# Kernel tuning notes

Measured on AMD Instinct MI355X. Metric: run time of the kernel, lower is better.

Reference implementation:

```python
import jax, jax.numpy as jnp
import numpy as np

N, LN, S, T = 50000, 64, 8, 4
E = 800000
MU = 0.9


def setup_inputs() -> dict:
    key = jax.random.key(0)
    ks = jax.random.split(key, 10)
    X_Node = jax.random.randint(ks[0], (E,), 0, N, dtype=jnp.int64) if jax.config.jax_enable_x64 else jax.random.randint(ks[0], (E,), 0, N).astype(jnp.int32)
    X_Neis = jax.random.randint(ks[1], (E,), 0, N).astype(X_Node.dtype)
    dg_list = jax.random.randint(ks[2], (E,), 1, 64).astype(jnp.float32)
    sc = 0.05
    W_emb = jax.random.normal(ks[3], (N, LN), jnp.float32) * sc
    Wxi = jax.random.normal(ks[4], (2 * LN, S * S), jnp.float32) * sc
    bxi = jnp.zeros((S * S,), jnp.float32)
    Wrou = jax.random.normal(ks[5], (LN, S), jnp.float32) * sc
    brou = jnp.zeros((S,), jnp.float32)
    Wout = jax.random.normal(ks[6], (LN + S, 3), jnp.float32) * sc
    bout = jnp.zeros((3,), jnp.float32)
    return {"X_Node": X_Node, "X_Neis": X_Neis, "dg_list": dg_list,
            "W_emb": W_emb, "Wxi": Wxi, "bxi": bxi,
            "Wrou": Wrou, "brou": brou, "Wout": Wout, "bout": bout}


def reference(X_Node, X_Neis, dg_list, W_emb, Wxi, bxi, Wrou, brou, Wout, bout):
    # Edge-wise feature gather: X = [emb[src] || emb[dst]]  -> [E, 2*LN]
    node_e = W_emb[X_Node]
    neis_e = W_emb[X_Neis]
    X = jnp.concatenate([node_e, neis_e], axis=1)
    # Hw precompute (loop-invariant): A [E,S,S], b [E,S]
    A = jnp.tanh(X @ Wxi + bxi).reshape(-1, S, S) * (MU / S) / dg_list[:, None, None]
    b = jnp.tanh(node_e @ Wrou + brou)

    states = jnp.zeros((N, S), dtype=W_emb.dtype)

    def step(states, _):
        H = states[X_Node]                      # gather [E, S]
        H = jnp.einsum('eij,ej->ei', A, H) + b  # per-edge small matvec
        # AggrSum's one-hot [V,E] matmul == scatter-add by X_Node
        new_states = jax.ops.segment_sum(H, X_Node, num_segments=N)
        return new_states, None

    states, _ = jax.lax.scan(step, states, None, length=T)
    logits = jnp.concatenate([W_emb, states], axis=1) @ Wout + bout
    return jax.nn.softmax(logits, axis=1)
```

## Files before the change

### kernel.cpp

```cpp
#include <hip/hip_runtime.h>
#include <hip/hip_fp16.h>
#include <math.h>

#define N_NODES 50000
#define LNDIM   64
#define E_EDGES 800000
#define MU_OVER_S 0.1125f
#define HPAD 16
#define NRANGE 8
#define RANGE_SZ ((N_NODES + NRANGE - 1) / NRANGE)
#define MAXDEG 48
#define PRE_TPB 128
#define PRE_TILES ((N_NODES + PRE_TPB - 1) / PRE_TPB)
#define LDS_STRIDE 129

__device__ __forceinline__ unsigned short f2bf(float f) {
    unsigned int u = __float_as_uint(f);
    u = (u + 0x7FFFu + ((u >> 16) & 1u)) >> 16;
    return (unsigned short)u;
}
__device__ __forceinline__ float bf2f(unsigned short b) {
    return __uint_as_float((unsigned)b << 16);
}
__device__ __forceinline__ float h2f(unsigned short h) {
    __half_raw hr; hr.x = h;
    return __half2float(__half(hr));
}
__device__ __forceinline__ float poly_tanh(float x) {
    float x2 = x * x;
    float a  = fmaf(x2, 0.13333333333f, -0.33333333333f);
    return fmaf(x * x2, a, x);
}

__global__ __launch_bounds__(256) void zero_kernel(int4* __restrict__ p, int n4)
{
    int i = blockIdx.x * 256 + threadIdx.x;
    if (i < n4) p[i] = make_int4(0, 0, 0, 0);
}

__global__ __launch_bounds__(PRE_TPB, 4) void precompute_kernel(
    const float* __restrict__ W_emb, const float* __restrict__ Wxi,
    const float* __restrict__ bxi,   const float* __restrict__ Wrou,
    const float* __restrict__ brou,
    unsigned short* __restrict__ T1, unsigned short* __restrict__ U,
    float* __restrict__ Bv)
{
    __shared__ float ldsT[32 * LDS_STRIDE];
    int pass = blockIdx.x / PRE_TILES;
    int tile = blockIdx.x % PRE_TILES;
    int tid  = threadIdx.x;
    int base = tile * PRE_TPB;
    int v    = base + tid;

    if (pass == 4) {
        float acc[8];
        #pragma unroll
        for (int j = 0; j < 8; ++j) acc[j] = brou[j];
        for (int kc = 0; kc < 2; ++kc) {
            __syncthreads();
            #pragma unroll
            for (int c = 0; c < 8; ++c) {
                int idx  = c * PRE_TPB + tid;
                int node = idx >> 3, part = idx & 7;
                int nn   = min(base + node, N_NODES - 1);
                float4 q = *(const float4*)(W_emb + (size_t)nn * 64 + kc * 32 + part * 4);
                ldsT[(part*4+0)*LDS_STRIDE + node] = q.x;
                ldsT[(part*4+1)*LDS_STRIDE + node] = q.y;
                ldsT[(part*4+2)*LDS_STRIDE + node] = q.z;
                ldsT[(part*4+3)*LDS_STRIDE + node] = q.w;
            }
            __syncthreads();
            for (int kk = 0; kk < 32; ++kk) {
                float ek = ldsT[kk * LDS_STRIDE + tid];
                const float* wr = Wrou + (kc*32 + kk) * 8;
                #pragma unroll
                for (int j = 0; j < 8; ++j) acc[j] = fmaf(ek, wr[j], acc[j]);
            }
        }
        if (v < N_NODES) {
            float4* dst = (float4*)(Bv + (size_t)v * 8);
            dst[0] = make_float4(tanhf(acc[0]), tanhf(acc[1]), tanhf(acc[2]), tanhf(acc[3]));
            dst[1] = make_float4(tanhf(acc[4]), tanhf(acc[5]), tanhf(acc[6]), tanhf(acc[7]));
        }
        return;
    }

    int is_u  = pass >> 1;
    int jbase = (pass & 1) * 32;
    const float* W = Wxi + (is_u ? 64 * 64 : 0) + jbase;
    float acc[32];
    if (is_u) {
        #pragma unroll
        for (int j = 0; j < 32; ++j) acc[j] = 0.f;
    } else {
        #pragma unroll
        for (int j = 0; j < 32; ++j) acc[j] = bxi[jbase + j];
    }
    for (int kc = 0; kc < 2; ++kc) {
        __syncthreads();
        #pragma unroll
        for (int c = 0; c < 8; ++c) {
            int idx  = c * PRE_TPB + tid;
            int node = idx >> 3, part = idx & 7;
            int nn   = min(base + node, N_NODES - 1);
            float4 q = *(const float4*)(W_emb + (size_t)nn * 64 + kc * 32 + part * 4);
            ldsT[(part*4+0)*LDS_STRIDE + node] = q.x;
            ldsT[(part*4+1)*LDS_STRIDE + node] = q.y;
            ldsT[(part*4+2)*LDS_STRIDE + node] = q.z;
            ldsT[(part*4+3)*LDS_STRIDE + node] = q.w;
        }
        __syncthreads();
        for (int kk = 0; kk < 32; ++kk) {
            float ek = ldsT[kk * LDS_STRIDE + tid];
            const float* wr = W + (kc*32 + kk) * 64;
            #pragma unroll
            for (int j = 0; j < 32; ++j) acc[j] = fmaf(ek, wr[j], acc[j]);
        }
    }
    if (v >= N_NODES) return;
    unsigned short* outp = is_u ? U : T1;
    uint4* dst = (uint4*)(outp + (size_t)v * 64 + jbase);
    #pragma unroll
    for (int t = 0; t < 4; ++t) {
        uint4 q;
        q.x = (unsigned)f2bf(acc[8*t+0]) | ((unsigned)f2bf(acc[8*t+1]) << 16);
        q.y = (unsigned)f2bf(acc[8*t+2]) | ((unsigned)f2bf(acc[8*t+3]) << 16);
        q.z = (unsigned)f2bf(acc[8*t+4]) | ((unsigned)f2bf(acc[8*t+5]) << 16);
        q.w = (unsigned)f2bf(acc[8*t+6]) | ((unsigned)f2bf(acc[8*t+7]) << 16);
        dst[t] = q;
    }
}

__global__ __launch_bounds__(256) void scatter_kernel(
    const int* __restrict__ X_Node, const int* __restrict__ X_Neis,
    const float* __restrict__ dg_list, int* __restrict__ cnt_arr,
    unsigned* __restrict__ pk_s)
{
    int r = blockIdx.x & (NRANGE - 1);
    int e = (blockIdx.x >> 3) * 256 + threadIdx.x;
    if (e >= E_EDGES) return;
    int node = X_Node[e];
    if (node < r * RANGE_SZ || node >= (r + 1) * RANGE_SZ) return;
    unsigned nei = (unsigned)X_Neis[e];
    float    sc  = MU_OVER_S / dg_list[e];
    __half_raw hr = __half_raw(__float2half(sc));
    unsigned hb  = (unsigned)hr.x;
    int pos = atomicAdd(&cnt_arr[(size_t)node * HPAD], 1);
    if (pos < MAXDEG) pk_s[(size_t)node * MAXDEG + pos] = nei | (hb << 16);
}

__global__ __launch_bounds__(256, 4) void main_kernel(
    const float* __restrict__ W_emb, const float* __restrict__ Wout,
    const float* __restrict__ bout,
    const unsigned short* __restrict__ T1, const unsigned short* __restrict__ U,
    const float* __restrict__ Bv, const int* __restrict__ cnt_arr,
    const unsigned* __restrict__ pk_s, float* __restrict__ out)
{
    int lane = threadIdx.x & 63;
    int wid  = threadIdx.x >> 6;
    int v    = blockIdx.x * 4 + wid;
    if (v >= N_NODES) return;

    int cntv = min(cnt_arr[(size_t)v * HPAD], MAXDEG);
    unsigned pk = (lane < MAXDEG) ? pk_s[(size_t)v * MAXDEG + lane] : 0u;
    float t = bf2f(T1[(size_t)v * 64 + lane]);

    float m0 = 0.f, m1 = 0.f, m2 = 0.f, m3 = 0.f;
    int cnt4 = (cntv + 3) & ~3;

    if (cnt4 > 0) {
        unsigned cq0 = (unsigned)__builtin_amdgcn_readlane((int)pk, 0);
        unsigned cq1 = (unsigned)__builtin_amdgcn_readlane((int)pk, 1);
        unsigned cq2 = (unsigned)__builtin_amdgcn_readlane((int)pk, 2);
        unsigned cq3 = (unsigned)__builtin_amdgcn_readlane((int)pk, 3);
        float cu0 = bf2f(U[(size_t)(cq0 & 0xFFFFu) * 64 + lane]);
        float cu1 = bf2f(U[(size_t)(cq1 & 0xFFFFu) * 64 + lane]);
        float cu2 = bf2f(U[(size_t)(cq2 & 0xFFFFu) * 64 + lane]);
        float cu3 = bf2f(U[(size_t)(cq3 & 0xFFFFu) * 64 + lane]);

        for (int k = 0; k < cnt4; k += 4) {
            int kn = (k + 4 < cnt4) ? k + 4 : 0;
            unsigned nq0 = (unsigned)__builtin_amdgcn_readlane((int)pk, kn + 0);
            unsigned nq1 = (unsigned)__builtin_amdgcn_readlane((int)pk, kn + 1);
            unsigned nq2 = (unsigned)__builtin_amdgcn_readlane((int)pk, kn + 2);
            unsigned nq3 = (unsigned)__builtin_amdgcn_readlane((int)pk, kn + 3);
            float nu0 = bf2f(U[(size_t)(nq0 & 0xFFFFu) * 64 + lane]);
            float nu1 = bf2f(U[(size_t)(nq1 & 0xFFFFu) * 64 + lane]);
            float nu2 = bf2f(U[(size_t)(nq2 & 0xFFFFu) * 64 + lane]);
            float nu3 = bf2f(U[(size_t)(nq3 & 0xFFFFu) * 64 + lane]);

            float g0 = poly_tanh(t + cu0) * h2f((unsigned short)(cq0 >> 16));
            float g1 = poly_tanh(t + cu1) * h2f((unsigned short)(cq1 >> 16));
            float g2 = poly_tanh(t + cu2) * h2f((unsigned short)(cq2 >> 16));
            float g3 = poly_tanh(t + cu3) * h2f((unsigned short)(cq3 >> 16));
            m0 += (k + 0 < cntv) ? g0 : 0.f;
            m1 += (k + 1 < cntv) ? g1 : 0.f;
            m2 += (k + 2 < cntv) ? g2 : 0.f;
            m3 += (k + 3 < cntv) ? g3 : 0.f;

            cq0 = nq0; cq1 = nq1; cq2 = nq2; cq3 = nq3;
            cu0 = nu0; cu1 = nu1; cu2 = nu2; cu3 = nu3;
        }
    }
    float macc = (m0 + m1) + (m2 + m3);

    int   j   = lane & 7;
    int   i   = lane >> 3;
    float cnt = (float)cntv;
    float cj  = cnt * Bv[v * 8 + j];
    float ci  = __shfl(cj, i);
    float sj  = cj;

    #pragma unroll
    for (int step = 0; step < 3; ++step) {
        float p = macc * sj;
        p += __shfl_xor(p, 1);
        p += __shfl_xor(p, 2);
        p += __shfl_xor(p, 4);
        float snew = p + ci;
        sj = __shfl(snew, j * 8);
    }

    float emb = W_emb[(size_t)v * 64 + lane];
    float p0 = emb * Wout[lane * 3 + 0];
    float p1 = emb * Wout[lane * 3 + 1];
    float p2 = emb * Wout[lane * 3 + 2];
    if (lane < 8) {
        p0 = fmaf(sj, Wout[(64 + lane) * 3 + 0], p0);
        p1 = fmaf(sj, Wout[(64 + lane) * 3 + 1], p1);
        p2 = fmaf(sj, Wout[(64 + lane) * 3 + 2], p2);
    }
    #pragma unroll
    for (int m = 1; m < 64; m <<= 1) {
        p0 += __shfl_xor(p0, m);
        p1 += __shfl_xor(p1, m);
        p2 += __shfl_xor(p2, m);
    }
    float L0 = p0 + bout[0], L1 = p1 + bout[1], L2 = p2 + bout[2];
    float mx = fmaxf(L0, fmaxf(L1, L2));
    float e0 = expf(L0 - mx), e1 = expf(L1 - mx), e2 = expf(L2 - mx);
    float inv = 1.f / (e0 + e1 + e2);
    float rr = (lane == 0) ? e0 : (lane == 1 ? e1 : e2);
    if (lane < 3) out[v * 3 + lane] = rr * inv;
}

extern "C" void kernel_launch(void* const* d_in, const int* in_sizes, int n_in,
                              void* d_out, int out_size, void* d_ws, size_t ws_size,
                              hipStream_t stream)
{
    const int*   X_Node = (const int*)  d_in[0];
    const int*   X_Neis = (const int*)  d_in[1];
    const float* dg     = (const float*)d_in[2];
    const float* W_emb  = (const float*)d_in[3];
    const float* Wxi    = (const float*)d_in[4];
    const float* bxi    = (const float*)d_in[5];
    const float* Wrou   = (const float*)d_in[6];
    const float* brou   = (const float*)d_in[7];
    const float* Wout   = (const float*)d_in[8];
    const float* bout   = (const float*)d_in[9];
    float*       out    = (float*)d_out;

    char*  ws  = (char*)d_ws;
    size_t off = 0;
    auto alloc = [&](size_t bytes) -> void* {
        void* p = ws + off;
        off += (bytes + 255) & ~(size_t)255;
        return p;
    };
    unsigned short* T1      = (unsigned short*)alloc((size_t)N_NODES * 64 * 2);
    unsigned short* U       = (unsigned short*)alloc((size_t)N_NODES * 64 * 2);
    float*          Bv      = (float*)alloc((size_t)N_NODES * 8 * 4);
    int*            cnt_arr = (int*)  alloc((size_t)N_NODES * HPAD * 4);
    unsigned*       pk_s    = (unsigned*)alloc(((size_t)N_NODES * MAXDEG + 64) * 4);

    const int NBE = (E_EDGES + 255) / 256;
    const int NZ4 = N_NODES * HPAD / 4;

    zero_kernel<<<(NZ4 + 255) / 256, 256, 0, stream>>>((int4*)cnt_arr, NZ4);
    precompute_kernel<<<PRE_TILES * 5, PRE_TPB, 0, stream>>>(
        W_emb, Wxi, bxi, Wrou, brou, T1, U, Bv);
    scatter_kernel<<<NBE * NRANGE, 256, 0, stream>>>(
        X_Node, X_Neis, dg, cnt_arr, pk_s);
    main_kernel<<<(N_NODES + 3) / 4, 256, 0, stream>>>(
        W_emb, Wout, bout, T1, U, Bv, cnt_arr, pk_s, out);
}
```

Baseline: 110.5 us.

## Two-pass bucketed edge scatter and 16-wide batched neighbor gathers

The edge scatter used to re-read every edge in 8 node-range passes. It now runs one bucketing pass that writes (node, payload) pairs into 8 per-range buckets using block-local LDS counts and one global atomic per bucket. A second pass does the per-node atomic placement from those buckets, which aims to cut redundant edge reads and improve atomic locality. The main kernel's gather loop now issues 16 U loads before any compute, separated by a sched_barrier, to raise memory-level parallelism at the cost of more registers. Bucket overflow past BCAP drops edges silently, and the readlane reads past cntv depend on the padded pk_s tail.

```diff
diff --git a/kernel.cpp b/kernel.cpp
--- a/kernel.cpp
+++ b/kernel.cpp
@@ -10,6 +10,7 @@
 #define NRANGE 8
 #define RANGE_SZ ((N_NODES + NRANGE - 1) / NRANGE)
 #define MAXDEG 48
+#define BCAP 110000
 #define PRE_TPB 128
 #define PRE_TILES ((N_NODES + PRE_TPB - 1) / PRE_TPB)
 #define LDS_STRIDE 129
@@ -131,22 +132,42 @@
     }
 }
 
-__global__ __launch_bounds__(256) void scatter_kernel(
+__global__ __launch_bounds__(256) void bucket_kernel(
     const int* __restrict__ X_Node, const int* __restrict__ X_Neis,
-    const float* __restrict__ dg_list, int* __restrict__ cnt_arr,
-    unsigned* __restrict__ pk_s)
-{
-    int r = blockIdx.x & (NRANGE - 1);
-    int e = (blockIdx.x >> 3) * 256 + threadIdx.x;
-    if (e >= E_EDGES) return;
+    const float* __restrict__ dg_list, int* __restrict__ bkt_cursor,
+    uint2* __restrict__ pairs)
+{
+    __shared__ int cnt[NRANGE];
+    __shared__ int basep[NRANGE];
+    int tid = threadIdx.x;
+    int e   = blockIdx.x * 256 + tid;
+    if (tid < NRANGE) cnt[tid] = 0;
+    __syncthreads();
+
     int node = X_Node[e];
-    if (node < r * RANGE_SZ || node >= (r + 1) * RANGE_SZ) return;
     unsigned nei = (unsigned)X_Neis[e];
     float    sc  = MU_OVER_S / dg_list[e];
     __half_raw hr = __half_raw(__float2half(sc));
-    unsigned hb  = (unsigned)hr.x;
-    int pos = atomicAdd(&cnt_arr[(size_t)node * HPAD], 1);
-    if (pos < MAXDEG) pk_s[(size_t)node * MAXDEG + pos] = nei | (hb << 16);
+    unsigned py  = nei | ((unsigned)hr.x << 16);
+    int r    = node / RANGE_SZ;
+    int rank = atomicAdd(&cnt[r], 1);
+    __syncthreads();
+    if (tid < NRANGE) basep[tid] = atomicAdd(&bkt_cursor[tid * HPAD], cnt[tid]);
+    __syncthreads();
+    int pos = basep[r] + rank;
+    if (pos < BCAP) pairs[(size_t)r * BCAP + pos] = make_uint2((unsigned)node, py);
+}
+
+__global__ __launch_bounds__(256) void scatter2_kernel(
+    const uint2* __restrict__ pairs, const int* __restrict__ bkt_cursor,
+    int* __restrict__ cnt_arr, unsigned* __restrict__ pk_s)
+{
+    int r = blockIdx.x & (NRANGE - 1);
+    int i = (blockIdx.x >> 3) * 256 + threadIdx.x;
+    if (i >= bkt_cursor[r * HPAD]) return;
+    uint2 p = pairs[(size_t)r * BCAP + i];
+    int pos = atomicAdd(&cnt_arr[(size_t)p.x * HPAD], 1);
+    if (pos < MAXDEG) pk_s[(size_t)p.x * MAXDEG + pos] = p.y;
 }
 
 __global__ __launch_bounds__(256, 4) void main_kernel(
@@ -166,40 +187,24 @@
     float t = bf2f(T1[(size_t)v * 64 + lane]);
 
     float m0 = 0.f, m1 = 0.f, m2 = 0.f, m3 = 0.f;
-    int cnt4 = (cntv + 3) & ~3;
-
-    if (cnt4 > 0) {
-        unsigned cq0 = (unsigned)__builtin_amdgcn_readlane((int)pk, 0);
-        unsigned cq1 = (unsigned)__builtin_amdgcn_readlane((int)pk, 1);
-        unsigned cq2 = (unsigned)__builtin_amdgcn_readlane((int)pk, 2);
-        unsigned cq3 = (unsigned)__builtin_amdgcn_readlane((int)pk, 3);
-        float cu0 = bf2f(U[(size_t)(cq0 & 0xFFFFu) * 64 + lane]);
-        float cu1 = bf2f(U[(size_t)(cq1 & 0xFFFFu) * 64 + lane]);
-        float cu2 = bf2f(U[(size_t)(cq2 & 0xFFFFu) * 64 + lane]);
-        float cu3 = bf2f(U[(size_t)(cq3 & 0xFFFFu) * 64 + lane]);
-
-        for (int k = 0; k < cnt4; k += 4) {
-            int kn = (k + 4 < cnt4) ? k + 4 : 0;
-            unsigned nq0 = (unsigned)__builtin_amdgcn_readlane((int)pk, kn + 0);
-            unsigned nq1 = (unsigned)__builtin_amdgcn_readlane((int)pk, kn + 1);
-            unsigned nq2 = (unsigned)__builtin_amdgcn_readlane((int)pk, kn + 2);
-            unsigned nq3 = (unsigned)__builtin_amdgcn_readlane((int)pk, kn + 3);
-            float nu0 = bf2f(U[(size_t)(nq0 & 0xFFFFu) * 64 + lane]);
-            float nu1 = bf2f(U[(size_t)(nq1 & 0xFFFFu) * 64 + lane]);
-            float nu2 = bf2f(U[(size_t)(nq2 & 0xFFFFu) * 64 + lane]);
-            float nu3 = bf2f(U[(size_t)(nq3 & 0xFFFFu) * 64 + lane]);
-
-            float g0 = poly_tanh(t + cu0) * h2f((unsigned short)(cq0 >> 16));
-            float g1 = poly_tanh(t + cu1) * h2f((unsigned short)(cq1 >> 16));
-            float g2 = poly_tanh(t + cu2) * h2f((unsigned short)(cq2 >> 16));
-            float g3 = poly_tanh(t + cu3) * h2f((unsigned short)(cq3 >> 16));
-            m0 += (k + 0 < cntv) ? g0 : 0.f;
-            m1 += (k + 1 < cntv) ? g1 : 0.f;
-            m2 += (k + 2 < cntv) ? g2 : 0.f;
-            m3 += (k + 3 < cntv) ? g3 : 0.f;
-
-            cq0 = nq0; cq1 = nq1; cq2 = nq2; cq3 = nq3;
-            cu0 = nu0; cu1 = nu1; cu2 = nu2; cu3 = nu3;
+
+    for (int k0 = 0; k0 < cntv; k0 += 16) {
+        unsigned q[16];
+        float    u[16];
+        #pragma unroll
+        for (int x = 0; x < 16; ++x) {
+            q[x] = (unsigned)__builtin_amdgcn_readlane((int)pk, k0 + x);
+            u[x] = bf2f(U[(size_t)(q[x] & 0xFFFFu) * 64 + lane]);
+        }
+        __builtin_amdgcn_sched_barrier(0);
+        #pragma unroll
+        for (int x = 0; x < 16; ++x) {
+            float g = poly_tanh(t + u[x]) * h2f((unsigned short)(q[x] >> 16));
+            float gm = (k0 + x < cntv) ? g : 0.f;
+            if      ((x & 3) == 0) m0 += gm;
+            else if ((x & 3) == 1) m1 += gm;
+            else if ((x & 3) == 2) m2 += gm;
+            else                   m3 += gm;
         }
     }
     float macc = (m0 + m1) + (m2 + m3);
@@ -267,20 +272,23 @@
         off += (bytes + 255) & ~(size_t)255;
         return p;
     };
-    unsigned short* T1      = (unsigned short*)alloc((size_t)N_NODES * 64 * 2);
-    unsigned short* U       = (unsigned short*)alloc((size_t)N_NODES * 64 * 2);
-    float*          Bv      = (float*)alloc((size_t)N_NODES * 8 * 4);
-    int*            cnt_arr = (int*)  alloc((size_t)N_NODES * HPAD * 4);
-    unsigned*       pk_s    = (unsigned*)alloc(((size_t)N_NODES * MAXDEG + 64) * 4);
-
-    const int NBE = (E_EDGES + 255) / 256;
-    const int NZ4 = N_NODES * HPAD / 4;
+    unsigned short* T1       = (unsigned short*)alloc((size_t)N_NODES * 64 * 2);
+    unsigned short* U        = (unsigned short*)alloc((size_t)N_NODES * 64 * 2);
+    float*          Bv       = (float*)alloc((size_t)N_NODES * 8 * 4);
+    int*            cnt_arr  = (int*)  alloc((size_t)N_NODES * HPAD * 4);
+    int*            bkt_cur  = (int*)  alloc((size_t)NRANGE * HPAD * 4);
+    uint2*          pairs    = (uint2*)alloc((size_t)NRANGE * BCAP * 8);
+    unsigned*       pk_s     = (unsigned*)alloc(((size_t)N_NODES * MAXDEG + 64) * 4);
+
+    const int NBE = E_EDGES / 256;
+    const int NZ4 = (N_NODES * HPAD + NRANGE * HPAD) / 4;
 
     zero_kernel<<<(NZ4 + 255) / 256, 256, 0, stream>>>((int4*)cnt_arr, NZ4);
     precompute_kernel<<<PRE_TILES * 5, PRE_TPB, 0, stream>>>(
         W_emb, Wxi, bxi, Wrou, brou, T1, U, Bv);
-    scatter_kernel<<<NBE * NRANGE, 256, 0, stream>>>(
-        X_Node, X_Neis, dg, cnt_arr, pk_s);
+    bucket_kernel<<<NBE, 256, 0, stream>>>(X_Node, X_Neis, dg, bkt_cur, pairs);
+    scatter2_kernel<<<((BCAP + 255) / 256) * NRANGE, 256, 0, stream>>>(
+        pairs, bkt_cur, cnt_arr, pk_s);
     main_kernel<<<(N_NODES + 3) / 4, 256, 0, stream>>>(
         W_emb, Wout, bout, T1, U, Bv, cnt_arr, pk_s, out);
 }
```

Result: slower. 173.6 us (+57.0%).
